# Kernel optimization log

Measured on AMD Instinct MI355X. Metric: run time of the kernel, lower is better.

## Reference

```python
import jax, jax.numpy as jnp
import numpy as np

BS, S, D, H = 4, 1024, 768, 12
NE, M, P = 42, 8, 500
IN_C, OUT_C = 3, 256
EMB, BLK, NL = 768, 64, 97


def setup_inputs() -> dict:
    key = jax.random.key(0)
    ks = jax.random.split(key, 16)
    seq_out = jax.random.normal(ks[0], (BS, S, D), jnp.float32)
    attention = jax.random.uniform(ks[1], (BS, H, S, S), jnp.float32)
    ent_tok = jax.random.randint(ks[2], (BS, NE, M), 0, 1022)
    ent_mask = (jax.random.uniform(ks[3], (BS, NE, M)) < 0.7).astype(jnp.float32)
    ent_mask = ent_mask.at[:, :, 0].set(1.0)  # every entity has >=1 mention
    hts = jax.random.randint(ks[4], (BS, P, 2), 0, NE)
    sc = 0.02
    return {
        'seq_out': seq_out,
        'attention': attention,
        'ent_tok': ent_tok,
        'ent_mask': ent_mask,
        'hts': hts,
        'W_liner': jax.random.normal(ks[5], (D, IN_C)) * sc,
        'b_liner': jnp.zeros((IN_C,), jnp.float32),
        'W_seg': jax.random.normal(ks[6], (IN_C, OUT_C)) * sc,
        'b_seg': jnp.zeros((OUT_C,), jnp.float32),
        'W_head': jax.random.normal(ks[7], (D + OUT_C, EMB)) * sc,
        'b_head': jnp.zeros((EMB,), jnp.float32),
        'W_tail': jax.random.normal(ks[8], (D + OUT_C, EMB)) * sc,
        'b_tail': jnp.zeros((EMB,), jnp.float32),
        'W_bil': jax.random.normal(ks[9], (EMB * BLK, NL)) * sc,
        'b_bil': jnp.zeros((NL,), jnp.float32),
    }


def reference(seq_out, attention, ent_tok, ent_mask, hts,
              W_liner, b_liner, W_seg, b_seg,
              W_head, b_head, W_tail, b_tail, W_bil, b_bil):
    bs, S_, d = seq_out.shape
    heads = attention.shape[1]
    # --- get_hrt: per-entity ragged pooling (offset=1 on token starts) ---
    idx = jnp.clip(ent_tok + 1, 0, S_ - 1)                   # [bs,ne,M]
    valid = ent_mask * (ent_tok + 1 < S_).astype(ent_mask.dtype)
    b_ix = jnp.arange(bs)[:, None, None]
    tok_emb = seq_out[b_ix, idx]                             # [bs,ne,M,d]
    neg = jnp.where(valid[..., None] > 0, tok_emb, jnp.float32(-1e30))
    e_emb = jax.nn.logsumexp(neg, axis=2)                    # [bs,ne,d]
    cnt = valid.sum(2)                                       # [bs,ne]
    e_emb = jnp.where((cnt > 0)[..., None], e_emb, 0.0)
    att_g = attention[b_ix, :, idx]                          # [bs,ne,M,H,S]
    e_att = (att_g * valid[..., None, None]).sum(2) / jnp.maximum(cnt, 1.0)[..., None, None]  # [bs,ne,H,S]
    e_att = jnp.where((cnt > 0)[..., None, None], e_att, 0.0)
    # --- get_channel_map: attention-weighted context contraction ---
    ht_att = jnp.einsum('bihs,bjhs->bijs', e_att, e_att) / heads  # [bs,ne,ne,S]
    ht_att = ht_att / (ht_att.sum(-1, keepdims=True) + 1e-5)
    feat = jnp.einsum('bijs,bsd->bijd', ht_att, seq_out)          # [bs,ne,ne,d]
    # --- liner + segmentation stand-in (pointwise) ---
    attn_map = (feat @ W_liner + b_liner) @ W_seg + b_seg         # [bs,ne,ne,OUT_C]
    # --- gather pair features ---
    bp = jnp.arange(bs)[:, None]
    h_i, t_i = hts[..., 0], hts[..., 1]
    h_t = attn_map[bp, h_i, t_i].reshape(-1, attn_map.shape[-1])  # [bs*P,OUT_C]
    hs = e_emb[bp, h_i].reshape(-1, d)
    ts = e_emb[bp, t_i].reshape(-1, d)
    hs = jnp.tanh(jnp.concatenate([hs, h_t], axis=1) @ W_head + b_head)
    ts = jnp.tanh(jnp.concatenate([ts, h_t], axis=1) @ W_tail + b_tail)
    # --- block bilinear classifier ---
    n = hs.shape[0]
    b1 = hs.reshape(n, EMB // BLK, BLK)
    b2 = ts.reshape(n, EMB // BLK, BLK)
    bl = (b1[:, :, :, None] * b2[:, :, None, :]).reshape(n, EMB * BLK)
    logits = bl @ W_bil + b_bil                                   # [bs*P, NL]
    return logits
```

## Files before the change

### kernel.cpp

```cpp
#include <hip/hip_runtime.h>
#include <hip/hip_bf16.h>
#include <math.h>

#define BSZ 4
#define SEQ 1024
#define DIM 768
#define NH 12
#define NEnt 42
#define MM 8
#define PPairs 500
#define INC 3
#define OUTC 256
#define EMB 768
#define BLKsz 64
#define NL 97
#define NPAIR (BSZ*PPairs)
#define XROWS 2048
#define NCHUNK 24

typedef __bf16 bf16x8 __attribute__((ext_vector_type(8)));
typedef __bf16 bf16x4 __attribute__((ext_vector_type(4)));
typedef float f32x4 __attribute__((ext_vector_type(4)));

#define OFF_EEMB  4096
#define OFF_EATT  520192
#define OFF_SP    4648960
#define OFF_XB    4698112
#define OFF_WHT   13086720
#define OFF_WT    16232448
#define OFF_HSB   25767936
#define OFF_TSB   28839936
#define OFF_PART  31911936

#define B_EEMB0 0
#define B_EATT0 168
#define B_SP0   2184
#define B_WHT0  3208
#define B_WT0   3592
#define B_ZERO0 4360
#define B_TOTAL 4362

__device__ __forceinline__ float ldin(const void* p, long long i, int f32) {
  if (f32) return ((const float*)p)[i];
  unsigned int u = (unsigned int)(((const unsigned short*)p)[i]) << 16;
  union { unsigned int u; float f; } c; c.u = u;
  return c.f;
}

__device__ __forceinline__ f32x4 ldin4(const void* p, long long i, int f32) {
  f32x4 r;
  if (f32) {
    r = *(const f32x4*)((const float*)p + i);
  } else {
    unsigned long long v = *(const unsigned long long*)((const unsigned short*)p + i);
    union { unsigned int u; float f; } c;
    c.u = (unsigned int)(v & 0xFFFFu) << 16;         r[0] = c.f;
    c.u = (unsigned int)((v >> 16) & 0xFFFFu) << 16; r[1] = c.f;
    c.u = (unsigned int)((v >> 32) & 0xFFFFu) << 16; r[2] = c.f;
    c.u = (unsigned int)((v >> 48) & 0xFFFFu) << 16; r[3] = c.f;
  }
  return r;
}

__device__ __forceinline__ float tanhf_fast(float x) {
  float ax = fabsf(x);
  float t = __expf(-2.0f*ax);
  float r = (1.0f - t)/(1.0f + t);
  return x < 0.0f ? -r : r;
}

__global__ void k_detect(const void* w_head, int* flag) {
  int tid = threadIdx.x;
  unsigned int word = ((const unsigned int*)w_head)[tid];
  union { unsigned int u; float f; } c;
  c.u = (word & 0xFFFFu) << 16;
  float v = fabsf(c.f);
  unsigned long long m = __ballot(v > 1.0f);
  if (tid == 0) flag[0] = (__popcll(m) >= 8) ? 1 : 0;
}

__global__ __launch_bounds__(256)
void k_stage1(const void* seq, const void* att, const int* etok,
              const void* emask, const void* wliner,
              const void* whead, const void* wtail, const void* wbil,
              const int* flag,
              float* e_emb, __bf16* e_att, float* sp,
              __bf16* whT, __bf16* wT, __bf16* Xb) {
  __shared__ float smem[64*98];
  int blk = blockIdx.x;
  int tid = threadIdx.x;
  int f32 = *flag;

  if (blk < B_EATT0) {
    int be = blk, b = be / NEnt;
    int* sidx = (int*)smem;
    float* sval = smem + 16;
    if (tid < MM) {
      int t = etok[be*MM + tid];
      int ip = t + 1;
      float v = ldin(emask, be*MM + tid, f32);
      sval[tid] = (ip < SEQ) ? v : 0.0f;
      sidx[tid] = ip < 0 ? 0 : (ip > SEQ-1 ? SEQ-1 : ip);
    }
    __syncthreads();
    float cnt = 0.0f;
#pragma unroll
    for (int m = 0; m < MM; m++) cnt += sval[m];
    for (int d = tid; d < DIM; d += 256) {
      float x[MM];
#pragma unroll
      for (int m = 0; m < MM; m++)
        x[m] = ldin(seq, ((long long)(b*SEQ) + sidx[m])*DIM + d, f32);
      float mx = -1e30f;
#pragma unroll
      for (int m = 0; m < MM; m++) if (sval[m] > 0.0f && x[m] > mx) mx = x[m];
      float s = 0.0f;
#pragma unroll
      for (int m = 0; m < MM; m++) if (sval[m] > 0.0f) s += expf(x[m] - mx);
      e_emb[(long long)be*DIM + d] = (cnt > 0.0f) ? (mx + logf(s)) : 0.0f;
    }
  } else if (blk < B_SP0) {
    int t1 = blk - B_EATT0;
    int h = t1 % NH, be = t1 / NH, b = be / NEnt;
    int* sidx = (int*)smem;
    float* sval = smem + 16;
    if (tid < MM) {
      int t = etok[be*MM + tid];
      int ip = t + 1;
      float v = ldin(emask, be*MM + tid, f32);
      sval[tid] = (ip < SEQ) ? v : 0.0f;
      sidx[tid] = ip < 0 ? 0 : (ip > SEQ-1 ? SEQ-1 : ip);
    }
    __syncthreads();
    float cnt = 0.0f;
#pragma unroll
    for (int m = 0; m < MM; m++) cnt += sval[m];
    float rs = (cnt > 0.0f) ? 1.0f/fmaxf(cnt, 1.0f) : 0.0f;
    long long abase = ((long long)(b*NH + h))*SEQ*SEQ;
    int s0 = tid*4;
    f32x4 acc = (f32x4){0,0,0,0};
#pragma unroll
    for (int m = 0; m < MM; m++)
      if (sval[m] > 0.0f) {
        f32x4 v = ldin4(att, abase + (long long)sidx[m]*SEQ + s0, f32);
        acc += sval[m]*v;
      }
    bf16x4 ov;
#pragma unroll
    for (int k = 0; k < 4; k++) ov[k] = (__bf16)(acc[k]*rs);
    *(bf16x4*)(e_att + ((long long)(be*NH + h))*SEQ + s0) = ov;
  } else if (blk < B_WHT0) {
    int t2 = blk - B_SP0;
    int b = t2 >> 8;
    int wv = tid >> 6, l = tid & 63;
    int s = ((t2 & 255) << 2) + wv;
    long long rb = ((long long)(b*SEQ) + s)*DIM;
    float a0 = 0, a1 = 0, a2 = 0;
#pragma unroll
    for (int i = 0; i < DIM/64; i++) {
      int d = l + i*64;
      float x = ldin(seq, rb + d, f32);
      a0 += x*ldin(wliner, (long long)d*3 + 0, f32);
      a1 += x*ldin(wliner, (long long)d*3 + 1, f32);
      a2 += x*ldin(wliner, (long long)d*3 + 2, f32);
    }
#pragma unroll
    for (int o = 32; o; o >>= 1) {
      a0 += __shfl_down(a0, o);
      a1 += __shfl_down(a1, o);
      a2 += __shfl_down(a2, o);
    }
    if (l == 0) {
      sp[0*(BSZ*SEQ) + b*SEQ + s] = a0;
      sp[1*(BSZ*SEQ) + b*SEQ + s] = a1;
      sp[2*(BSZ*SEQ) + b*SEQ + s] = a2;
    }
  } else if (blk < B_WT0) {
    int t3 = blk - B_WHT0;
    int kb = t3 & 15, rest = t3 >> 4;
    int nb = rest % 12, y = rest / 12;
    const void* W = y ? wtail : whead;
    for (int i = tid; i < 64*64; i += 256) {
      int r = i >> 6, c = i & 63;
      smem[r*65 + c] = ldin(W, (long long)(kb*64 + r)*EMB + nb*64 + c, f32);
    }
    __syncthreads();
    for (int j = tid; j < 64*64; j += 256) {
      int r = j >> 6, k = j & 63;
      whT[((long long)y*EMB + nb*64 + r)*1024 + kb*64 + k] = (__bf16)smem[k*65 + r];
    }
  } else if (blk < B_ZERO0) {
    int t4 = blk - B_WT0;
    int kb = t4 & 63, g = t4 >> 6;
    long long base = ((long long)g*4096 + kb*64)*97;
    for (int i = tid; i < 64*97; i += 256)
      smem[(i/97)*98 + (i%97)] = ldin(wbil, base + i, f32);
    __syncthreads();
    for (int j = tid; j < 97*64; j += 256) {
      int l = j >> 6, k = j & 63;
      wT[((long long)g*97 + l)*4096 + kb*64 + k] = (__bf16)smem[k*98 + l];
    }
  } else {
    int y = blk - B_ZERO0;
    uint4 z = {0,0,0,0};
    uint4* dst = (uint4*)(Xb + ((long long)(y*XROWS + NPAIR))*1024);
    for (int i = tid; i < 48*1024*2/16; i += 256) dst[i] = z;
  }
}

__global__ __launch_bounds__(256)
void k_pair2(const __bf16* e_att, const float* sp, const float* e_emb,
             const int* hts, const void* bliner, const void* wseg,
             const void* bseg, const int* flag, __bf16* Xb) {
  __shared__ float cross[4][4];
  int p = blockIdx.x;
  int b = p / PPairs;
  int tid = threadIdx.x;
  int f32 = *flag;
  int hi = hts[p*2 + 0];
  int ti = hts[p*2 + 1];
  const __bf16* ei = e_att + ((long long)(b*NEnt + hi))*NH*SEQ;
  const __bf16* ej = e_att + ((long long)(b*NEnt + ti))*NH*SEQ;
  int s0 = tid*4;
  f32x4 q = (f32x4){0,0,0,0};
#pragma unroll
  for (int h = 0; h < NH; h++) {
    bf16x4 xi = *(const bf16x4*)(ei + h*SEQ + s0);
    bf16x4 xj = *(const bf16x4*)(ej + h*SEQ + s0);
#pragma unroll
    for (int k = 0; k < 4; k++) q[k] += (float)xi[k]*(float)xj[k];
  }
  f32x4 w0 = *(const f32x4*)(sp + 0*(BSZ*SEQ) + b*SEQ + s0);
  f32x4 w1 = *(const f32x4*)(sp + 1*(BSZ*SEQ) + b*SEQ + s0);
  f32x4 w2 = *(const f32x4*)(sp + 2*(BSZ*SEQ) + b*SEQ + s0);
  float dn = q[0]+q[1]+q[2]+q[3];
  float a0 = q[0]*w0[0]+q[1]*w0[1]+q[2]*w0[2]+q[3]*w0[3];
  float a1 = q[0]*w1[0]+q[1]*w1[1]+q[2]*w1[2]+q[3]*w1[3];
  float a2 = q[0]*w2[0]+q[1]*w2[1]+q[2]*w2[2]+q[3]*w2[3];
#pragma unroll
  for (int o = 32; o; o >>= 1) {
    dn += __shfl_down(dn, o);
    a0 += __shfl_down(a0, o);
    a1 += __shfl_down(a1, o);
    a2 += __shfl_down(a2, o);
  }
  int wv = tid >> 6, l = tid & 63;
  if (l == 0) { cross[0][wv] = dn; cross[1][wv] = a0; cross[2][wv] = a1; cross[3][wv] = a2; }
  __syncthreads();
  float DN = cross[0][0]+cross[0][1]+cross[0][2]+cross[0][3];
  float A0 = cross[1][0]+cross[1][1]+cross[1][2]+cross[1][3];
  float A1 = cross[2][0]+cross[2][1]+cross[2][2]+cross[2][3];
  float A2 = cross[3][0]+cross[3][1]+cross[3][2]+cross[3][3];
  const float inv = 1.0f/(float)NH;
  float scale = inv/(DN*inv + 1e-5f);
  float v0 = A0*scale + ldin(bliner, 0, f32);
  float v1 = A1*scale + ldin(bliner, 1, f32);
  float v2 = A2*scale + ldin(bliner, 2, f32);
  float o = ldin(bseg, tid, f32)
          + v0*ldin(wseg, 0*OUTC + tid, f32)
          + v1*ldin(wseg, 1*OUTC + tid, f32)
          + v2*ldin(wseg, 2*OUTC + tid, f32);
  __bf16* X0 = Xb + ((long long)(0*XROWS + p))*1024;
  __bf16* X1 = Xb + ((long long)(1*XROWS + p))*1024;
  X0[DIM + tid] = (__bf16)o;
  X1[DIM + tid] = (__bf16)o;
  const float* eh = e_emb + (long long)(b*NEnt + hi)*DIM;
  const float* et = e_emb + (long long)(b*NEnt + ti)*DIM;
  for (int k = tid; k < DIM; k += 256) {
    X0[k] = (__bf16)eh[k];
    X1[k] = (__bf16)et[k];
  }
}

__global__ __launch_bounds__(256, 1)
void k_htmm(const __bf16* Xb, const __bf16* whT,
            const void* bhead, const void* btail, const int* flag,
            __bf16* hsb, __bf16* tsb) {
  __shared__ __bf16 Xa[2][128][72];
  __shared__ __bf16 Bb[2][64][72];
  int tid = threadIdx.x;
  int w = tid >> 6, lane = tid & 63, quad = lane >> 4, col = lane & 15;
  int m0 = blockIdx.x*128;
  int n0 = blockIdx.y*64;
  int y  = blockIdx.z;
  int f32 = *flag;
  const __bf16* Xg = Xb + (long long)y*XROWS*1024;
  const __bf16* Wg = whT + ((long long)y*EMB + n0)*1024;

  auto stage = [&](int kk, int p) {
#pragma unroll
    for (int it = 0; it < 4; it++) {
      int r = (tid >> 3) + it*32;
      int c0 = (tid & 7)*8;
      bf16x8 v = *(const bf16x8*)(Xg + (long long)(m0 + r)*1024 + kk + c0);
      *(bf16x8*)&Xa[p][r][c0] = v;
    }
#pragma unroll
    for (int it = 0; it < 2; it++) {
      int r = (tid >> 3) + it*32;
      int c0 = (tid & 7)*8;
      bf16x8 v = *(const bf16x8*)(Wg + (long long)r*1024 + kk + c0);
      *(bf16x8*)&Bb[p][r][c0] = v;
    }
  };

  f32x4 acc[2][4];
#pragma unroll
  for (int mf = 0; mf < 2; mf++)
#pragma unroll
    for (int nt = 0; nt < 4; nt++) acc[mf][nt] = (f32x4){0,0,0,0};

  stage(0, 0);
  __syncthreads();
  for (int c = 0; c < 16; c++) {
    int p = c & 1;
    if (c + 1 < 16) stage((c+1)*64, p ^ 1);
#pragma unroll
    for (int s = 0; s < 2; s++) {
      bf16x8 av[2], bv[4];
#pragma unroll
      for (int mf = 0; mf < 2; mf++)
        av[mf] = *(bf16x8*)&Xa[p][w*32 + mf*16 + col][s*32 + quad*8];
#pragma unroll
      for (int nt = 0; nt < 4; nt++)
        bv[nt] = *(bf16x8*)&Bb[p][nt*16 + col][s*32 + quad*8];
#pragma unroll
      for (int mf = 0; mf < 2; mf++)
#pragma unroll
        for (int nt = 0; nt < 4; nt++)
          acc[mf][nt] = __builtin_amdgcn_mfma_f32_16x16x32_bf16(av[mf], bv[nt],
                                                                acc[mf][nt], 0, 0, 0);
    }
    __syncthreads();
  }

  const void* Bv = y ? btail : bhead;
  __bf16* out = y ? tsb : hsb;
#pragma unroll
  for (int nt = 0; nt < 4; nt++) {
    int n = n0 + nt*16 + col;
    float bias = ldin(Bv, n, f32);
#pragma unroll
    for (int mf = 0; mf < 2; mf++)
#pragma unroll
      for (int reg = 0; reg < 4; reg++) {
        int m = m0 + w*32 + mf*16 + quad*4 + reg;
        if (m < NPAIR)
          out[(long long)m*EMB + n] = (__bf16)tanhf_fast(acc[mf][nt][reg] + bias);
      }
  }
}

__global__ __launch_bounds__(128, 2)
void k_bilmfma(const __bf16* hsb, const __bf16* tsb,
               const __bf16* wT, _Float16* part24) {
  __shared__ __bf16 hslT[32][72];
  int tid = threadIdx.x;
  int w = tid >> 6, lane = tid & 63, quad = lane >> 4, col = lane & 15;
  int m0 = blockIdx.x*64;
  int c  = blockIdx.y;
  int g  = c >> 1, kh = c & 1;

  {
    int srow = tid & 63;
    int grow = m0 + srow; if (grow > NPAIR-1) grow = NPAIR-1;
    int ah = (tid >> 6)*16;
    const __bf16* hp = hsb + (long long)grow*EMB + g*BLKsz + kh*32 + ah;
#pragma unroll
    for (int c0 = 0; c0 < 2; c0++) {
      bf16x8 hv = *(const bf16x8*)(hp + c0*8);
#pragma unroll
      for (int j = 0; j < 8; j++) hslT[ah + c0*8 + j][srow] = hv[j];
    }
  }
  bf16x8 tsv[2][2];
#pragma unroll
  for (int mf = 0; mf < 2; mf++) {
    int row = m0 + w*32 + mf*16 + col; if (row > NPAIR-1) row = NPAIR-1;
    const __bf16* tp = tsb + (long long)row*EMB + g*BLKsz + quad*8;
    tsv[mf][0] = *(const bf16x8*)(tp);
    tsv[mf][1] = *(const bf16x8*)(tp + 32);
  }
  __syncthreads();

  const __bf16* wg = wT + (long long)g*NL*4096 + kh*2048 + quad*8;
  int boff[7];
#pragma unroll
  for (int nt = 0; nt < 7; nt++) {
    int l = nt*16 + col; if (l > 96) l = 96;
    boff[nt] = l*4096;
  }
  f32x4 acc[2][7];
#pragma unroll
  for (int mf = 0; mf < 2; mf++)
#pragma unroll
    for (int nt = 0; nt < 7; nt++) acc[mf][nt] = (f32x4){0,0,0,0};

  bf16x8 bv[2][7];
#pragma unroll
  for (int nt = 0; nt < 7; nt++) bv[0][nt] = *(const bf16x8*)(wg + boff[nt]);
#pragma unroll
  for (int nt = 0; nt < 7; nt++) bv[1][nt] = *(const bf16x8*)(wg + boff[nt] + 32);

  for (int a = 0; a < 32; a++) {
    float hv[2];
#pragma unroll
    for (int mf = 0; mf < 2; mf++)
      hv[mf] = (float)hslT[a][w*32 + mf*16 + col];
#pragma unroll
    for (int half = 0; half < 2; half++) {
      bf16x8 af[2];
#pragma unroll
      for (int mf = 0; mf < 2; mf++)
#pragma unroll
        for (int j = 0; j < 8; j++)
          af[mf][j] = (__bf16)(hv[mf] * (float)tsv[mf][half][j]);
#pragma unroll
      for (int mf = 0; mf < 2; mf++)
#pragma unroll
        for (int nt = 0; nt < 7; nt++)
          acc[mf][nt] = __builtin_amdgcn_mfma_f32_16x16x32_bf16(af[mf], bv[half][nt],
                                                                acc[mf][nt], 0, 0, 0);
      int knext = (a+1)*64 + half*32;
      if (knext >= 2048) knext = a*64 + half*32;
#pragma unroll
      for (int nt = 0; nt < 7; nt++)
        bv[half][nt] = *(const bf16x8*)(wg + boff[nt] + knext);
    }
  }

  _Float16* ps = part24 + (long long)c*NPAIR*NL;
#pragma unroll
  for (int mf = 0; mf < 2; mf++)
#pragma unroll
    for (int nt = 0; nt < 7; nt++)
#pragma unroll
      for (int reg = 0; reg < 4; reg++) {
        int n = m0 + w*32 + mf*16 + quad*4 + reg;
        int l = nt*16 + col;
        if (n < NPAIR && l < NL)
          ps[(long long)n*NL + l] = (_Float16)acc[mf][nt][reg];
      }
}

__global__ void k_final(const _Float16* part24, const void* b_bil, const int* flag,
                        void* out) {
  int i = blockIdx.x*256 + threadIdx.x;
  if (i >= NPAIR*NL) return;
  int l = i % NL;
  int f32 = *flag;
  float v = ldin(b_bil, l, f32);
#pragma unroll
  for (int c = 0; c < NCHUNK; c++) v += (float)part24[(long long)c*NPAIR*NL + i];
  if (f32) ((float*)out)[i] = v;
  else ((__hip_bfloat16*)out)[i] = __float2bfloat16(v);
}

extern "C" void kernel_launch(void* const* d_in, const int* in_sizes, int n_in,
                              void* d_out, int out_size, void* d_ws, size_t ws_size,
                              hipStream_t stream) {
  const void* seq    = d_in[0];
  const void* att    = d_in[1];
  const int*  etok   = (const int*)d_in[2];
  const void* emask  = d_in[3];
  const int*  hts    = (const int*)d_in[4];
  const void* wliner = d_in[5];
  const void* bliner = d_in[6];
  const void* wseg   = d_in[7];
  const void* bseg   = d_in[8];
  const void* whead  = d_in[9];
  const void* bhead  = d_in[10];
  const void* wtail  = d_in[11];
  const void* btail  = d_in[12];
  const void* wbil   = d_in[13];
  const void* bbil   = d_in[14];

  char* ws = (char*)d_ws;
  int*      flag   = (int*)ws;
  float*    e_emb  = (float*)(ws + OFF_EEMB);
  __bf16*   e_att  = (__bf16*)(ws + OFF_EATT);
  float*    sp     = (float*)(ws + OFF_SP);
  __bf16*   Xb     = (__bf16*)(ws + OFF_XB);
  __bf16*   whT    = (__bf16*)(ws + OFF_WHT);
  __bf16*   wT     = (__bf16*)(ws + OFF_WT);
  __bf16*   hsb    = (__bf16*)(ws + OFF_HSB);
  __bf16*   tsb    = (__bf16*)(ws + OFF_TSB);
  _Float16* part24 = (_Float16*)(ws + OFF_PART);

  k_detect<<<1, 64, 0, stream>>>(whead, flag);
  k_stage1<<<B_TOTAL, 256, 0, stream>>>(seq, att, etok, emask, wliner,
                                        whead, wtail, wbil, flag,
                                        e_emb, e_att, sp, whT, wT, Xb);
  k_pair2<<<NPAIR, 256, 0, stream>>>(e_att, sp, e_emb, hts, bliner, wseg, bseg,
                                     flag, Xb);
  k_htmm<<<dim3(16, 12, 2), 256, 0, stream>>>(Xb, whT, bhead, btail, flag, hsb, tsb);
  k_bilmfma<<<dim3(32, NCHUNK), 128, 0, stream>>>(hsb, tsb, wT, part24);
  k_final<<<(NPAIR*NL + 255)/256, 256, 0, stream>>>(part24, bbil, flag, d_out);
}
```

Measured before the change: 418.9 us.

## Fold dtype detection into stage1 and vectorize pair, pooling, final loads

Drops the separate detect launch by having every stage1 block recompute the dtype flag from the head weights, with block 0 writing it for later kernels. The entity pooling, the pair gather and the final reduction switch to 4- or 8-wide vector loads and stores. The pair kernel splits the 12 heads across two thread halves with 8-element bf16 loads. Each stage1 block now pays an extra global read and a barrier. The f16x4 loads in the final kernel assume suitable alignment, and the element count NPAIR*NL is divisible by 4.

New measurement: 416.3 us. Within noise of the previous version (-0.6%).

```diff
diff --git a/kernel.cpp b/kernel.cpp
--- a/kernel.cpp
+++ b/kernel.cpp
@@ -21,6 +21,7 @@
 typedef __bf16 bf16x8 __attribute__((ext_vector_type(8)));
 typedef __bf16 bf16x4 __attribute__((ext_vector_type(4)));
 typedef float f32x4 __attribute__((ext_vector_type(4)));
+typedef _Float16 f16x4 __attribute__((ext_vector_type(4)));
 
 #define OFF_EEMB  4096
 #define OFF_EATT  520192
@@ -69,27 +70,27 @@
   return x < 0.0f ? -r : r;
 }
 
-__global__ void k_detect(const void* w_head, int* flag) {
-  int tid = threadIdx.x;
-  unsigned int word = ((const unsigned int*)w_head)[tid];
-  union { unsigned int u; float f; } c;
-  c.u = (word & 0xFFFFu) << 16;
-  float v = fabsf(c.f);
-  unsigned long long m = __ballot(v > 1.0f);
-  if (tid == 0) flag[0] = (__popcll(m) >= 8) ? 1 : 0;
-}
-
 __global__ __launch_bounds__(256)
 void k_stage1(const void* seq, const void* att, const int* etok,
               const void* emask, const void* wliner,
               const void* whead, const void* wtail, const void* wbil,
-              const int* flag,
+              int* flagOut,
               float* e_emb, __bf16* e_att, float* sp,
               __bf16* whT, __bf16* wT, __bf16* Xb) {
   __shared__ float smem[64*98];
+  __shared__ int sflag;
   int blk = blockIdx.x;
   int tid = threadIdx.x;
-  int f32 = *flag;
+
+  if (tid < 64) {
+    unsigned int word = ((const unsigned int*)whead)[tid];
+    union { unsigned int u; float f; } c; c.u = (word & 0xFFFFu) << 16;
+    unsigned long long m = __ballot(fabsf(c.f) > 1.0f);
+    if (tid == 0) sflag = (__popcll(m) >= 8) ? 1 : 0;
+  }
+  __syncthreads();
+  const int f32 = sflag;
+  if (blk == 0 && tid == 0) flagOut[0] = f32;
 
   if (blk < B_EATT0) {
     int be = blk, b = be / NEnt;
@@ -106,18 +107,24 @@
     float cnt = 0.0f;
 #pragma unroll
     for (int m = 0; m < MM; m++) cnt += sval[m];
-    for (int d = tid; d < DIM; d += 256) {
-      float x[MM];
+    if (tid < 192) {
+      int d0 = tid*4;
+      f32x4 x[MM];
 #pragma unroll
       for (int m = 0; m < MM; m++)
-        x[m] = ldin(seq, ((long long)(b*SEQ) + sidx[m])*DIM + d, f32);
-      float mx = -1e30f;
-#pragma unroll
-      for (int m = 0; m < MM; m++) if (sval[m] > 0.0f && x[m] > mx) mx = x[m];
-      float s = 0.0f;
-#pragma unroll
-      for (int m = 0; m < MM; m++) if (sval[m] > 0.0f) s += expf(x[m] - mx);
-      e_emb[(long long)be*DIM + d] = (cnt > 0.0f) ? (mx + logf(s)) : 0.0f;
+        x[m] = ldin4(seq, ((long long)(b*SEQ) + sidx[m])*DIM + d0, f32);
+      f32x4 outv;
+#pragma unroll
+      for (int j = 0; j < 4; j++) {
+        float mx = -1e30f;
+#pragma unroll
+        for (int m = 0; m < MM; m++) if (sval[m] > 0.0f && x[m][j] > mx) mx = x[m][j];
+        float s = 0.0f;
+#pragma unroll
+        for (int m = 0; m < MM; m++) if (sval[m] > 0.0f) s += expf(x[m][j] - mx);
+        outv[j] = (cnt > 0.0f) ? (mx + logf(s)) : 0.0f;
+      }
+      *(f32x4*)(e_emb + (long long)be*DIM + d0) = outv;
     }
   } else if (blk < B_SP0) {
     int t1 = blk - B_EATT0;
@@ -209,9 +216,9 @@
 }
 
 __global__ __launch_bounds__(256)
-void k_pair2(const __bf16* e_att, const float* sp, const float* e_emb,
-             const int* hts, const void* bliner, const void* wseg,
-             const void* bseg, const int* flag, __bf16* Xb) {
+void k_pair(const __bf16* e_att, const float* sp, const float* e_emb,
+            const int* hts, const void* bliner, const void* wseg,
+            const void* bseg, const int* flag, __bf16* Xb) {
   __shared__ float cross[4][4];
   int p = blockIdx.x;
   int b = p / PPairs;
@@ -221,22 +228,34 @@
   int ti = hts[p*2 + 1];
   const __bf16* ei = e_att + ((long long)(b*NEnt + hi))*NH*SEQ;
   const __bf16* ej = e_att + ((long long)(b*NEnt + ti))*NH*SEQ;
-  int s0 = tid*4;
-  f32x4 q = (f32x4){0,0,0,0};
-#pragma unroll
-  for (int h = 0; h < NH; h++) {
-    bf16x4 xi = *(const bf16x4*)(ei + h*SEQ + s0);
-    bf16x4 xj = *(const bf16x4*)(ej + h*SEQ + s0);
-#pragma unroll
-    for (int k = 0; k < 4; k++) q[k] += (float)xi[k]*(float)xj[k];
-  }
-  f32x4 w0 = *(const f32x4*)(sp + 0*(BSZ*SEQ) + b*SEQ + s0);
-  f32x4 w1 = *(const f32x4*)(sp + 1*(BSZ*SEQ) + b*SEQ + s0);
-  f32x4 w2 = *(const f32x4*)(sp + 2*(BSZ*SEQ) + b*SEQ + s0);
-  float dn = q[0]+q[1]+q[2]+q[3];
-  float a0 = q[0]*w0[0]+q[1]*w0[1]+q[2]*w0[2]+q[3]*w0[3];
-  float a1 = q[0]*w1[0]+q[1]*w1[1]+q[2]*w1[2]+q[3]*w1[3];
-  float a2 = q[0]*w2[0]+q[1]*w2[1]+q[2]*w2[2]+q[3]*w2[3];
+  int hh = tid >> 7;
+  int st = tid & 127;
+  int s0 = st*8;
+  float q[8];
+#pragma unroll
+  for (int k = 0; k < 8; k++) q[k] = 0.0f;
+#pragma unroll
+  for (int hq = 0; hq < 6; hq++) {
+    int h = hh*6 + hq;
+    bf16x8 xi = *(const bf16x8*)(ei + h*SEQ + s0);
+    bf16x8 xj = *(const bf16x8*)(ej + h*SEQ + s0);
+#pragma unroll
+    for (int k = 0; k < 8; k++) q[k] += (float)xi[k]*(float)xj[k];
+  }
+  f32x4 w0a = *(const f32x4*)(sp + 0*(BSZ*SEQ) + b*SEQ + s0);
+  f32x4 w0b = *(const f32x4*)(sp + 0*(BSZ*SEQ) + b*SEQ + s0 + 4);
+  f32x4 w1a = *(const f32x4*)(sp + 1*(BSZ*SEQ) + b*SEQ + s0);
+  f32x4 w1b = *(const f32x4*)(sp + 1*(BSZ*SEQ) + b*SEQ + s0 + 4);
+  f32x4 w2a = *(const f32x4*)(sp + 2*(BSZ*SEQ) + b*SEQ + s0);
+  f32x4 w2b = *(const f32x4*)(sp + 2*(BSZ*SEQ) + b*SEQ + s0 + 4);
+  float dn = 0, a0 = 0, a1 = 0, a2 = 0;
+#pragma unroll
+  for (int k = 0; k < 4; k++) {
+    dn += q[k] + q[k+4];
+    a0 += q[k]*w0a[k] + q[k+4]*w0b[k];
+    a1 += q[k]*w1a[k] + q[k+4]*w1b[k];
+    a2 += q[k]*w2a[k] + q[k+4]*w2b[k];
+  }
 #pragma unroll
   for (int o = 32; o; o >>= 1) {
     dn += __shfl_down(dn, o);
@@ -266,9 +285,15 @@
   X1[DIM + tid] = (__bf16)o;
   const float* eh = e_emb + (long long)(b*NEnt + hi)*DIM;
   const float* et = e_emb + (long long)(b*NEnt + ti)*DIM;
-  for (int k = tid; k < DIM; k += 256) {
-    X0[k] = (__bf16)eh[k];
-    X1[k] = (__bf16)et[k];
+  if (tid < 192) {
+    int k0 = tid*4;
+    f32x4 vh = *(const f32x4*)(eh + k0);
+    f32x4 vt = *(const f32x4*)(et + k0);
+    bf16x4 oh, ot;
+#pragma unroll
+    for (int j = 0; j < 4; j++) { oh[j] = (__bf16)vh[j]; ot[j] = (__bf16)vt[j]; }
+    *(bf16x4*)(X0 + k0) = oh;
+    *(bf16x4*)(X1 + k0) = ot;
   }
 }
 
@@ -445,15 +470,26 @@
 
 __global__ void k_final(const _Float16* part24, const void* b_bil, const int* flag,
                         void* out) {
-  int i = blockIdx.x*256 + threadIdx.x;
-  if (i >= NPAIR*NL) return;
-  int l = i % NL;
+  int i4 = (blockIdx.x*256 + threadIdx.x)*4;
+  if (i4 >= NPAIR*NL) return;
   int f32 = *flag;
-  float v = ldin(b_bil, l, f32);
-#pragma unroll
-  for (int c = 0; c < NCHUNK; c++) v += (float)part24[(long long)c*NPAIR*NL + i];
-  if (f32) ((float*)out)[i] = v;
-  else ((__hip_bfloat16*)out)[i] = __float2bfloat16(v);
+  f32x4 v;
+#pragma unroll
+  for (int j = 0; j < 4; j++) v[j] = ldin(b_bil, (i4 + j) % NL, f32);
+#pragma unroll
+  for (int c = 0; c < NCHUNK; c++) {
+    f16x4 pv = *(const f16x4*)(part24 + (long long)c*NPAIR*NL + i4);
+#pragma unroll
+    for (int j = 0; j < 4; j++) v[j] += (float)pv[j];
+  }
+  if (f32) {
+    *(f32x4*)((float*)out + i4) = v;
+  } else {
+    bf16x4 ov;
+#pragma unroll
+    for (int j = 0; j < 4; j++) ov[j] = (__bf16)v[j];
+    *(bf16x4*)((__hip_bfloat16*)out + i4) = ov;
+  }
 }
 
 extern "C" void kernel_launch(void* const* d_in, const int* in_sizes, int n_in,
@@ -487,13 +523,12 @@
   __bf16*   tsb    = (__bf16*)(ws + OFF_TSB);
   _Float16* part24 = (_Float16*)(ws + OFF_PART);
 
-  k_detect<<<1, 64, 0, stream>>>(whead, flag);
   k_stage1<<<B_TOTAL, 256, 0, stream>>>(seq, att, etok, emask, wliner,
                                         whead, wtail, wbil, flag,
                                         e_emb, e_att, sp, whT, wT, Xb);
-  k_pair2<<<NPAIR, 256, 0, stream>>>(e_att, sp, e_emb, hts, bliner, wseg, bseg,
-                                     flag, Xb);
+  k_pair<<<NPAIR, 256, 0, stream>>>(e_att, sp, e_emb, hts, bliner, wseg, bseg,
+                                    flag, Xb);
   k_htmm<<<dim3(16, 12, 2), 256, 0, stream>>>(Xb, whT, bhead, btail, flag, hsb, tsb);
   k_bilmfma<<<dim3(32, NCHUNK), 128, 0, stream>>>(hsb, tsb, wT, part24);
-  k_final<<<(NPAIR*NL + 255)/256, 256, 0, stream>>>(part24, bbil, flag, d_out);
-}
+  k_final<<<(NPAIR*NL/4 + 255)/256, 256, 0, stream>>>(part24, bbil, flag, d_out);
+}
```
